# Performance work log

Hardware: AMD Instinct MI355X
Metric: run time of the kernel (lower is better)

## Reference

```python
import jax, jax.numpy as jnp
import numpy as np

L, H, D, FF, T, S, N = 4, 16, 1024, 4096, 256, 256, 16
NEG = -1e9

def layer_norm(x, g, b):
    mu = jnp.mean(x, axis=-1, keepdims=True)
    var = jnp.var(x, axis=-1, keepdims=True)
    return (x - mu) / jnp.sqrt(var + 1e-5) * g + b

def mha(q_in, k_in, v_in, wq, bq, wk, bk, wv, bv, wo, bo, mask):
    # q_in: [T,N,D]; k_in/v_in: [S,N,D]
    t, n, d = q_in.shape
    s = k_in.shape[0]
    hd = d // H
    scale = hd ** -0.5
    q = (q_in @ wq.T + bq) * scale
    k = k_in @ wk.T + bk
    v = v_in @ wv.T + bv
    q = q.reshape(t, n, H, hd)
    k = k.reshape(s, n, H, hd)
    v = v.reshape(s, n, H, hd)
    scores = jnp.einsum('tnhd,snhd->nhts', q, k)  # [N,H,T,S]
    if mask is not None:
        scores = scores + mask  # mask [T,S] broadcasts
    a = jax.nn.softmax(scores, axis=-1)
    o = jnp.einsum('nhts,snhd->tnhd', a, v).reshape(t, n, d)
    return o @ wo.T + bo

def forward(tgt, memory, sa_wq, sa_bq, sa_wk, sa_bk, sa_wv, sa_bv, sa_wo, sa_bo,
            ca_wq, ca_bq, ca_wk, ca_bk, ca_wv, ca_bv, ca_wo, ca_bo,
            w1, b1, w2, b2, ln1_g, ln1_b, ln2_g, ln2_b, ln3_g, ln3_b, lnf_g, lnf_b):
    t = tgt.shape[0]
    causal = jnp.where(jnp.triu(jnp.ones((t, t), bool), 1), jnp.float32(NEG), jnp.float32(0.0))
    x = tgt
    for i in range(L):
        sa = mha(x, x, x, sa_wq[i], sa_bq[i], sa_wk[i], sa_bk[i], sa_wv[i], sa_bv[i], sa_wo[i], sa_bo[i], causal)
        x = layer_norm(x + sa, ln1_g[i], ln1_b[i])
        ca = mha(x, memory, memory, ca_wq[i], ca_bq[i], ca_wk[i], ca_bk[i], ca_wv[i], ca_bv[i], ca_wo[i], ca_bo[i], None)
        x = layer_norm(x + ca, ln2_g[i], ln2_b[i])
        ff = jax.nn.relu(x @ w1[i].T + b1[i]) @ w2[i].T + b2[i]
        x = layer_norm(x + ff, ln3_g[i], ln3_b[i])
    return layer_norm(x, lnf_g, lnf_b)

def setup_inputs() -> dict:
    key = jax.random.key(0)
    ks = iter(jax.random.split(key, 40))
    def nrm(shape, s):
        return (jax.random.normal(next(ks), shape, jnp.float32) * s).astype(jnp.float32)
    sd = D ** -0.5
    inp = {
        'tgt': nrm((T, N, D), 1.0),
        'memory': nrm((S, N, D), 1.0),
    }
    for pre in ('sa', 'ca'):
        for nm in ('wq', 'wk', 'wv', 'wo'):
            inp[f'{pre}_{nm}'] = nrm((L, D, D), sd)
        for nm in ('bq', 'bk', 'bv', 'bo'):
            inp[f'{pre}_{nm}'] = jnp.zeros((L, D), jnp.float32)
    inp['w1'] = nrm((L, FF, D), sd)
    inp['b1'] = jnp.zeros((L, FF), jnp.float32)
    inp['w2'] = nrm((L, D, FF), FF ** -0.5)
    inp['b2'] = jnp.zeros((L, D), jnp.float32)
    for nm in ('ln1', 'ln2', 'ln3'):
        inp[f'{nm}_g'] = jnp.ones((L, D), jnp.float32)
        inp[f'{nm}_b'] = jnp.zeros((L, D), jnp.float32)
    inp['lnf_g'] = jnp.ones((D,), jnp.float32)
    inp['lnf_b'] = jnp.zeros((D,), jnp.float32)
    return inp

def reference(tgt, memory, sa_wq, sa_bq, sa_wk, sa_bk, sa_wv, sa_bv, sa_wo, sa_bo,
              ca_wq, ca_bq, ca_wk, ca_bk, ca_wv, ca_bv, ca_wo, ca_bo,
              w1, b1, w2, b2, ln1_g, ln1_b, ln2_g, ln2_b, ln3_g, ln3_b, lnf_g, lnf_b):
    return forward(tgt, memory, sa_wq, sa_bq, sa_wk, sa_bk, sa_wv, sa_bv, sa_wo, sa_bo,
                   ca_wq, ca_bq, ca_wk, ca_bk, ca_wv, ca_bv, ca_wo, ca_bo,
                   w1, b1, w2, b2, ln1_g, ln1_b, ln2_g, ln2_b, ln3_g, ln3_b, lnf_g, lnf_b)
```

## Files before the change

### kernel.cpp

```cpp
#include <hip/hip_runtime.h>


typedef __attribute__((ext_vector_type(4))) float f32x4;
typedef __attribute__((ext_vector_type(8))) short bf16x8;
typedef __attribute__((ext_vector_type(4))) unsigned short u16x4;
typedef __attribute__((ext_vector_type(4))) unsigned int   u32x4;

__device__ __forceinline__ unsigned short f2bf(float f) {
    unsigned int u = __builtin_bit_cast(unsigned int, f);
    u += 0x7fffu + ((u >> 16) & 1u);
    return (unsigned short)(u >> 16);
}

__device__ __forceinline__ void gll16(const unsigned short* g, unsigned short* l) {
    auto* gp = reinterpret_cast<const __attribute__((address_space(1))) unsigned int*>(
        reinterpret_cast<uintptr_t>(g));
    auto* lp = reinterpret_cast<__attribute__((address_space(3))) unsigned int*>(
        reinterpret_cast<uintptr_t>(l));
    __builtin_amdgcn_global_load_lds(gp, lp, 16, 0, 0);
}

__global__ __launch_bounds__(256, 4) void gemm128(
    const unsigned short* __restrict__ A,
    const unsigned short* __restrict__ Bw,
    const float* __restrict__ bias,
    unsigned short* __restrict__ outb,
    float* __restrict__ outf0,
    float* __restrict__ outf1,
    int N, int lda, int klen, int mode)
{
    __shared__ unsigned short Al[2][128 * 32];
    __shared__ unsigned short Bl[2][128 * 32];
    const int tid  = threadIdx.x;
    const int lane = tid & 63;
    const int w    = tid >> 6;
    const int wr   = (w >> 1) * 64;
    const int wc   = (w & 1) * 64;
    const int l15  = lane & 15;
    const int l4   = lane >> 4;

    const int gx   = gridDim.x;
    const int orig = blockIdx.y * gx + blockIdx.x;
    const int xcd  = orig & 7;
    const int lin  = orig >> 3;
    const int m0   = (xcd * 4 + (lin & 3)) * 128;
    const int n0   = (lin >> 2) * 128;
    const int kz   = blockIdx.z * klen;

    const int srow = w * 16 + (lane >> 2);
    const int scol = ((lane & 3) ^ ((srow >> 1) & 3)) * 8;
    const unsigned short* ag = A  + (size_t)(m0 + srow) * lda + kz + scol;
    const unsigned short* bg = Bw + (size_t)(n0 + srow) * lda + kz + scol;
    const size_t jstep = (size_t)64 * lda;
    const int lbase = (w * 16) * 32;

    int aoff[4], boff[4];
    #pragma unroll
    for (int i = 0; i < 4; ++i) {
        const int ra = wr + i * 16 + l15;
        const int rb = wc + i * 16 + l15;
        aoff[i] = ra * 32 + ((l4 ^ ((ra >> 1) & 3)) * 8);
        boff[i] = rb * 32 + ((l4 ^ ((rb >> 1) & 3)) * 8);
    }

    f32x4 acc[4][4];
    #pragma unroll
    for (int mi = 0; mi < 4; ++mi)
        #pragma unroll
        for (int ni = 0; ni < 4; ++ni)
            acc[mi][ni] = (f32x4){0.f, 0.f, 0.f, 0.f};

    #pragma unroll
    for (int j = 0; j < 2; ++j) {
        gll16(ag + j * jstep, &Al[0][lbase + j * 64 * 32]);
        gll16(bg + j * jstep, &Bl[0][lbase + j * 64 * 32]);
    }
    __syncthreads();

    const int nt = klen >> 5;
    int cur = 0;
    for (int t = 0; t < nt; ++t) {
        if (t + 1 < nt) {
            ag += 32; bg += 32;
            #pragma unroll
            for (int j = 0; j < 2; ++j) {
                gll16(ag + j * jstep, &Al[cur ^ 1][lbase + j * 64 * 32]);
                gll16(bg + j * jstep, &Bl[cur ^ 1][lbase + j * 64 * 32]);
            }
        }
        const unsigned short* ac = &Al[cur][0];
        const unsigned short* bc = &Bl[cur][0];
        bf16x8 af[4], bf[4];
        #pragma unroll
        for (int i = 0; i < 4; ++i) af[i] = *reinterpret_cast<const bf16x8*>(&ac[aoff[i]]);
        #pragma unroll
        for (int i = 0; i < 4; ++i) bf[i] = *reinterpret_cast<const bf16x8*>(&bc[boff[i]]);
        #pragma unroll
        for (int mi = 0; mi < 4; ++mi)
            #pragma unroll
            for (int ni = 0; ni < 4; ++ni)
                acc[mi][ni] = __builtin_amdgcn_mfma_f32_16x16x32_bf16(af[mi], bf[ni], acc[mi][ni], 0, 0, 0);
        __syncthreads();
        cur ^= 1;
    }

    float* po = (blockIdx.z == 0) ? outf0 : outf1;
    #pragma unroll
    for (int mi = 0; mi < 4; ++mi) {
        #pragma unroll
        for (int ni = 0; ni < 4; ++ni) {
            const int col = n0 + wc + ni * 16 + l15;
            const float bs = (mode == 3) ? 0.f : bias[col];
            #pragma unroll
            for (int r = 0; r < 4; ++r) {
                const int row = m0 + wr + mi * 16 + l4 * 4 + r;
                const float val = acc[mi][ni][r] + bs;
                if (mode == 0)      outb[(size_t)row * N + col] = f2bf(val);
                else if (mode == 1) outb[(size_t)row * N + col] = f2bf(fmaxf(val, 0.f));
                else                po[(size_t)row * N + col] = val;
            }
        }
    }
}

__global__ __launch_bounds__(256) void gemm_bt64(
    const unsigned short* __restrict__ A,
    const unsigned short* __restrict__ Bw,
    const float* __restrict__ bias,
    const float* __restrict__ resid,
    unsigned short* __restrict__ outb,
    float* __restrict__ outf,
    int M, int N, int K, int mode)
{
    __shared__ unsigned short Al[2][64 * 32];
    __shared__ unsigned short Bl[2][128 * 32];
    const int tid  = threadIdx.x;
    const int lane = tid & 63;
    const int w    = tid >> 6;
    const int wr   = (w >> 1) * 32;
    const int wc   = (w & 1) * 64;
    const int l15  = lane & 15;
    const int l4   = lane >> 4;

    const int gx = gridDim.x;
    const int orig = blockIdx.y * gx + blockIdx.x;
    const int xcd  = orig & 7;
    const int lin  = orig >> 3;
    const int m0   = (xcd * 8 + (lin & 7)) * 64;
    const int n0   = (lin >> 3) * 128;

    const int srow = w * 16 + (lane >> 2);
    const int scol = ((lane & 3) ^ ((srow >> 1) & 3)) * 8;
    const unsigned short* ag = A  + (size_t)(m0 + srow) * K + scol;
    const unsigned short* bg = Bw + (size_t)(n0 + srow) * K + scol;
    const size_t jstep = (size_t)64 * K;
    const int lbase = (w * 16) * 32;

    int aoff[2], boff[4];
    #pragma unroll
    for (int i = 0; i < 2; ++i) {
        const int ra = wr + i * 16 + l15;
        aoff[i] = ra * 32 + ((l4 ^ ((ra >> 1) & 3)) * 8);
    }
    #pragma unroll
    for (int i = 0; i < 4; ++i) {
        const int rb = wc + i * 16 + l15;
        boff[i] = rb * 32 + ((l4 ^ ((rb >> 1) & 3)) * 8);
    }

    f32x4 acc[2][4];
    #pragma unroll
    for (int mi = 0; mi < 2; ++mi)
        #pragma unroll
        for (int ni = 0; ni < 4; ++ni)
            acc[mi][ni] = (f32x4){0.f, 0.f, 0.f, 0.f};

    gll16(ag, &Al[0][lbase]);
    #pragma unroll
    for (int j = 0; j < 2; ++j) gll16(bg + j * jstep, &Bl[0][lbase + j * 64 * 32]);
    __syncthreads();

    const int nt = K >> 5;
    int cur = 0;
    for (int t = 0; t < nt; ++t) {
        if (t + 1 < nt) {
            ag += 32; bg += 32;
            gll16(ag, &Al[cur ^ 1][lbase]);
            #pragma unroll
            for (int j = 0; j < 2; ++j) gll16(bg + j * jstep, &Bl[cur ^ 1][lbase + j * 64 * 32]);
        }
        const unsigned short* ac = &Al[cur][0];
        const unsigned short* bc = &Bl[cur][0];
        bf16x8 af[2], bf[4];
        #pragma unroll
        for (int i = 0; i < 2; ++i) af[i] = *reinterpret_cast<const bf16x8*>(&ac[aoff[i]]);
        #pragma unroll
        for (int i = 0; i < 4; ++i) bf[i] = *reinterpret_cast<const bf16x8*>(&bc[boff[i]]);
        #pragma unroll
        for (int mi = 0; mi < 2; ++mi)
            #pragma unroll
            for (int ni = 0; ni < 4; ++ni)
                acc[mi][ni] = __builtin_amdgcn_mfma_f32_16x16x32_bf16(af[mi], bf[ni], acc[mi][ni], 0, 0, 0);
        __syncthreads();
        cur ^= 1;
    }

    #pragma unroll
    for (int mi = 0; mi < 2; ++mi) {
        #pragma unroll
        for (int ni = 0; ni < 4; ++ni) {
            const int col = n0 + wc + ni * 16 + l15;
            const float bs = bias[col];
            #pragma unroll
            for (int r = 0; r < 4; ++r) {
                const int row = m0 + wr + mi * 16 + l4 * 4 + r;
                const float val = acc[mi][ni][r] + bs;
                if (mode == 0) outb[(size_t)row * N + col] = f2bf(val);
                else           outf[(size_t)row * N + col] = val + resid[(size_t)row * N + col];
            }
        }
    }
}

__global__ __launch_bounds__(256) void attn_fused(
    const unsigned short* __restrict__ Q, int qs,
    const unsigned short* __restrict__ Kb, int ks_,
    const unsigned short* __restrict__ Vb, int vs,
    unsigned short* __restrict__ O,
    int causal)
{
    __shared__ unsigned short Kl[8][256][8];
    __shared__ unsigned short Vt[32][64][8];
    __shared__ unsigned short Pl[4][32][16][8];
    const int tid  = threadIdx.x;
    const int lane = tid & 63;
    const int w    = tid >> 6;
    const int n    = blockIdx.x >> 4;
    const int h    = blockIdx.x & 15;
    const int l15  = lane & 15;
    const int l4   = lane >> 4;
    const size_t hoff = (size_t)h * 64;

    #pragma unroll
    for (int i = 0; i < 8; ++i) {
        const int e = i * 256 + tid;
        const int s = e >> 3;
        const int c = e & 7;
        u32x4 kv = *reinterpret_cast<const u32x4*>(&Kb[((size_t)s * 16 + n) * ks_ + hoff + c * 8]);
        *reinterpret_cast<u32x4*>(&Kl[c][s][0]) = kv;
        u32x4 vv = *reinterpret_cast<const u32x4*>(&Vb[((size_t)s * 16 + n) * vs + hoff + c * 8]);
        const unsigned short* ve = reinterpret_cast<const unsigned short*>(&vv);
        #pragma unroll
        for (int j = 0; j < 8; ++j)
            Vt[s >> 3][c * 8 + j][s & 7] = ve[j];
    }
    __syncthreads();

    for (int ch = 0; ch < 4; ++ch) {
        const int t0 = w * 64 + ch * 16;
        bf16x8 qa[2];
        #pragma unroll
        for (int ks = 0; ks < 2; ++ks)
            qa[ks] = *reinterpret_cast<const bf16x8*>(
                &Q[((size_t)(t0 + l15) * 16 + n) * qs + hoff + ks * 32 + l4 * 8]);

        f32x4 sc[16];
        #pragma unroll
        for (int st = 0; st < 16; ++st) {
            f32x4 a = (f32x4){0.f, 0.f, 0.f, 0.f};
            #pragma unroll
            for (int ks = 0; ks < 2; ++ks) {
                bf16x8 kf = *reinterpret_cast<const bf16x8*>(&Kl[ks * 4 + l4][st * 16 + l15][0]);
                a = __builtin_amdgcn_mfma_f32_16x16x32_bf16(qa[ks], kf, a, 0, 0, 0);
            }
            sc[st] = a;
        }
        if (causal) {
            #pragma unroll
            for (int st = 0; st < 16; ++st) {
                const int sg = st * 16 + l15;
                #pragma unroll
                for (int r = 0; r < 4; ++r) {
                    const int tg = t0 + l4 * 4 + r;
                    if (sg > tg) sc[st][r] += -1e9f;
                }
            }
        }
        #pragma unroll
        for (int r = 0; r < 4; ++r) {
            float mx = -3.0e38f;
            #pragma unroll
            for (int st = 0; st < 16; ++st) mx = fmaxf(mx, sc[st][r]);
            #pragma unroll
            for (int dd = 1; dd < 16; dd <<= 1) mx = fmaxf(mx, __shfl_xor(mx, dd, 64));
            float sum = 0.f;
            #pragma unroll
            for (int st = 0; st < 16; ++st) {
                const float e = __expf(sc[st][r] - mx);
                sc[st][r] = e;
                sum += e;
            }
            #pragma unroll
            for (int dd = 1; dd < 16; dd <<= 1) sum += __shfl_xor(sum, dd, 64);
            const float inv = 1.f / sum;
            const int rl = l4 * 4 + r;
            #pragma unroll
            for (int st = 0; st < 16; ++st) {
                const int sg = st * 16 + l15;
                Pl[w][sg >> 3][rl][sg & 7] = f2bf(sc[st][r] * inv);
            }
        }
        f32x4 oacc[4];
        #pragma unroll
        for (int dt = 0; dt < 4; ++dt) oacc[dt] = (f32x4){0.f, 0.f, 0.f, 0.f};
        #pragma unroll
        for (int kt = 0; kt < 8; ++kt) {
            bf16x8 pa = *reinterpret_cast<const bf16x8*>(&Pl[w][kt * 4 + l4][l15][0]);
            #pragma unroll
            for (int dt = 0; dt < 4; ++dt) {
                bf16x8 vf = *reinterpret_cast<const bf16x8*>(&Vt[kt * 4 + l4][dt * 16 + l15][0]);
                oacc[dt] = __builtin_amdgcn_mfma_f32_16x16x32_bf16(pa, vf, oacc[dt], 0, 0, 0);
            }
        }
        #pragma unroll
        for (int dt = 0; dt < 4; ++dt)
            #pragma unroll
            for (int r = 0; r < 4; ++r)
                O[((size_t)(t0 + l4 * 4 + r) * 16 + n) * 1024 + hoff + dt * 16 + l15] = f2bf(oacc[dt][r]);
    }
}

__device__ __forceinline__ void ln_body(
    f32x4 (&v)[4], int row, int lane,
    const float* __restrict__ g, const float* __restrict__ b,
    float* __restrict__ xf, unsigned short* __restrict__ xb)
{
    float s = 0.f;
    #pragma unroll
    for (int i = 0; i < 4; ++i) s += v[i][0] + v[i][1] + v[i][2] + v[i][3];
    #pragma unroll
    for (int dd = 1; dd < 64; dd <<= 1) s += __shfl_xor(s, dd, 64);
    const float mu = s * (1.f / 1024.f);
    float q = 0.f;
    #pragma unroll
    for (int i = 0; i < 4; ++i)
        #pragma unroll
        for (int j = 0; j < 4; ++j) { const float d0 = v[i][j] - mu; q += d0 * d0; }
    #pragma unroll
    for (int dd = 1; dd < 64; dd <<= 1) q += __shfl_xor(q, dd, 64);
    const float rstd = rsqrtf(q * (1.f / 1024.f) + 1e-5f);
    #pragma unroll
    for (int i = 0; i < 4; ++i) {
        const int col = i * 256 + lane * 4;
        f32x4 gg = *reinterpret_cast<const f32x4*>(&g[col]);
        f32x4 bb = *reinterpret_cast<const f32x4*>(&b[col]);
        f32x4 y;
        #pragma unroll
        for (int j = 0; j < 4; ++j) y[j] = (v[i][j] - mu) * rstd * gg[j] + bb[j];
        if (xf) *reinterpret_cast<f32x4*>(&xf[(size_t)row * 1024 + col]) = y;
        if (xb) {
            u16x4 pk;
            #pragma unroll
            for (int j = 0; j < 4; ++j) pk[j] = f2bf(y[j]);
            *reinterpret_cast<u16x4*>(&xb[(size_t)row * 1024 + col]) = pk;
        }
    }
}

__global__ __launch_bounds__(256) void ln_kernel(
    const float* __restrict__ z, const float* __restrict__ g, const float* __restrict__ b,
    float* __restrict__ xf, unsigned short* __restrict__ xb)
{
    const int row  = blockIdx.x * 4 + (threadIdx.x >> 6);
    const int lane = threadIdx.x & 63;
    f32x4 v[4];
    #pragma unroll
    for (int i = 0; i < 4; ++i)
        v[i] = *reinterpret_cast<const f32x4*>(&z[(size_t)row * 1024 + i * 256 + lane * 4]);
    ln_body(v, row, lane, g, b, xf, xb);
}

__global__ __launch_bounds__(256) void ln_red2(
    const float* __restrict__ p0, const float* __restrict__ p1,
    const float* __restrict__ bias, const float* __restrict__ resid,
    const float* __restrict__ g, const float* __restrict__ b,
    float* __restrict__ xf, unsigned short* __restrict__ xb)
{
    const int row  = blockIdx.x * 4 + (threadIdx.x >> 6);
    const int lane = threadIdx.x & 63;
    f32x4 v[4];
    #pragma unroll
    for (int i = 0; i < 4; ++i) {
        const int col = i * 256 + lane * 4;
        const size_t o = (size_t)row * 1024 + col;
        f32x4 a0 = *reinterpret_cast<const f32x4*>(&p0[o]);
        f32x4 a1 = *reinterpret_cast<const f32x4*>(&p1[o]);
        f32x4 bs = *reinterpret_cast<const f32x4*>(&bias[col]);
        f32x4 rs = *reinterpret_cast<const f32x4*>(&resid[o]);
        v[i] = a0 + a1 + bs + rs;
    }
    ln_body(v, row, lane, g, b, xf, xb);
}

__global__ __launch_bounds__(256) void cvt_bf16(
    const float* __restrict__ in, unsigned short* __restrict__ out, int n)
{
    const int i = (blockIdx.x * 256 + threadIdx.x) * 4;
    if (i >= n) return;
    f32x4 v = *reinterpret_cast<const f32x4*>(&in[i]);
    u16x4 pk;
    #pragma unroll
    for (int j = 0; j < 4; ++j) pk[j] = f2bf(v[j]);
    *reinterpret_cast<u16x4*>(&out[i]) = pk;
}

__global__ __launch_bounds__(256) void pack_layer_w(
    const float* __restrict__ sa_wq, const float* __restrict__ sa_wk, const float* __restrict__ sa_wv,
    const float* __restrict__ ca_wq, const float* __restrict__ ca_wk, const float* __restrict__ ca_wv,
    const float* __restrict__ sa_wo, const float* __restrict__ ca_wo,
    const float* __restrict__ w1,   const float* __restrict__ w2,
    unsigned short* __restrict__ dst, int layer)
{
    const size_t DD = 1024u * 1024u;
    const size_t e  = ((size_t)blockIdx.x * 256 + threadIdx.x) * 4;
    const float* src;
    float scale = 1.f;
    if (e < 3 * DD) {
        const int part = (int)(e / DD);
        src = (part == 0 ? sa_wq : part == 1 ? sa_wk : sa_wv) + layer * DD + (e % DD);
        if (part == 0) scale = 0.125f;
    } else if (e < 6 * DD) {
        const size_t r = e - 3 * DD;
        const int part = (int)(r / DD);
        src = (part == 0 ? ca_wq : part == 1 ? ca_wk : ca_wv) + layer * DD + (r % DD);
        if (part == 0) scale = 0.125f;
    } else if (e < 7 * DD)  { src = sa_wo + layer * DD + (e - 6 * DD); }
    else if (e < 8 * DD)    { src = ca_wo + layer * DD + (e - 7 * DD); }
    else if (e < 12 * DD)   { src = w1 + (size_t)layer * 4 * DD + (e - 8 * DD); }
    else                    { src = w2 + (size_t)layer * 4 * DD + (e - 12 * DD); }
    f32x4 v = *reinterpret_cast<const f32x4*>(src);
    u16x4 pk;
    #pragma unroll
    for (int j = 0; j < 4; ++j) pk[j] = f2bf(v[j] * scale);
    *reinterpret_cast<u16x4*>(&dst[e]) = pk;
}

__global__ __launch_bounds__(256) void pack_bias(
    const float* __restrict__ sa_bq, const float* __restrict__ sa_bk, const float* __restrict__ sa_bv,
    const float* __restrict__ ca_bq, const float* __restrict__ ca_bk, const float* __restrict__ ca_bv,
    float* __restrict__ sab, float* __restrict__ cab)
{
    const int idx = blockIdx.x * 256 + threadIdx.x;
    const int half = idx / 12288;
    const int r    = idx % 12288;
    const int l    = r / 3072;
    const int pc   = r % 3072;
    const int part = pc >> 10;
    const int c    = pc & 1023;
    const float* src = half == 0 ? (part == 0 ? sa_bq : part == 1 ? sa_bk : sa_bv)
                                 : (part == 0 ? ca_bq : part == 1 ? ca_bk : ca_bv);
    const float v = src[l * 1024 + c] * (part == 0 ? 0.125f : 1.f);
    (half ? cab : sab)[l * 3072 + pc] = v;
}

extern "C" void kernel_launch(void* const* d_in, const int* in_sizes, int n_in,
                              void* d_out, int out_size, void* d_ws, size_t ws_size,
                              hipStream_t stream)
{
    (void)in_sizes; (void)n_in; (void)out_size; (void)ws_size;
    const int M  = 4096;
    const int Dm = 1024;
    const size_t DD = (size_t)Dm * Dm;

    const float* tgt   = (const float*)d_in[0];
    const float* mem   = (const float*)d_in[1];
    const float* sa_wq = (const float*)d_in[2];
    const float* sa_wk = (const float*)d_in[3];
    const float* sa_wv = (const float*)d_in[4];
    const float* sa_wo = (const float*)d_in[5];
    const float* sa_bq = (const float*)d_in[6];
    const float* sa_bk = (const float*)d_in[7];
    const float* sa_bv = (const float*)d_in[8];
    const float* sa_bo = (const float*)d_in[9];
    const float* ca_wq = (const float*)d_in[10];
    const float* ca_wk = (const float*)d_in[11];
    const float* ca_wv = (const float*)d_in[12];
    const float* ca_wo = (const float*)d_in[13];
    const float* ca_bq = (const float*)d_in[14];
    const float* ca_bk = (const float*)d_in[15];
    const float* ca_bv = (const float*)d_in[16];
    const float* ca_bo = (const float*)d_in[17];
    const float* w1    = (const float*)d_in[18];
    const float* b1    = (const float*)d_in[19];
    const float* w2    = (const float*)d_in[20];
    const float* b2    = (const float*)d_in[21];
    const float* ln1g  = (const float*)d_in[22];
    const float* ln1b  = (const float*)d_in[23];
    const float* ln2g  = (const float*)d_in[24];
    const float* ln2b  = (const float*)d_in[25];
    const float* ln3g  = (const float*)d_in[26];
    const float* ln3b  = (const float*)d_in[27];
    const float* lnfg  = (const float*)d_in[28];
    const float* lnfb  = (const float*)d_in[29];

    char* p = (char*)d_ws;
    float*          x_f    = (float*)p;          p += (size_t)M * Dm * 4;
    unsigned short* x_b    = (unsigned short*)p; p += (size_t)M * Dm * 2;
    unsigned short* mem_b  = (unsigned short*)p; p += (size_t)M * Dm * 2;
    unsigned short* qkv_b  = (unsigned short*)p; p += (size_t)M * 3072 * 2;
    unsigned short* cakv_b = (unsigned short*)p; p += (size_t)M * 2048 * 2;
    unsigned short* caq_b  = (unsigned short*)p; p += (size_t)M * Dm * 2;
    unsigned short* ao_b   = (unsigned short*)p; p += (size_t)M * Dm * 2;
    unsigned short* wpack  = (unsigned short*)p; p += 16 * DD * 2;
    float*          sab    = (float*)p;          p += 4 * 3072 * 4;
    float*          cab    = (float*)p;          p += 4 * 3072 * 4;
    unsigned short* h_b    = qkv_b;
    float*          par0   = (float*)((char*)qkv_b + (size_t)M * 4096 * 2);
    float*          par1   = (float*)wpack;
    float*          z_f    = (float*)d_out;

    dim3 blk(256);
    auto gemm64 = [&](const unsigned short* A, const unsigned short* Bw, const float* bias,
                      const float* resid, unsigned short* ob, float* of, int N, int K, int mode) {
        dim3 grid(N / 128, M / 64);
        gemm_bt64<<<grid, blk, 0, stream>>>(A, Bw, bias, resid, ob, of, M, N, K, mode);
    };

    cvt_bf16<<<4096, blk, 0, stream>>>(tgt, x_b, M * Dm);
    cvt_bf16<<<4096, blk, 0, stream>>>(mem, mem_b, M * Dm);
    pack_bias<<<96, blk, 0, stream>>>(sa_bq, sa_bk, sa_bv, ca_bq, ca_bk, ca_bv, sab, cab);

    const float* res = tgt;
    for (int i = 0; i < 4; ++i) {
        pack_layer_w<<<16384, blk, 0, stream>>>(sa_wq, sa_wk, sa_wv, ca_wq, ca_wk, ca_wv,
                                                sa_wo, ca_wo, w1, w2, wpack, i);
        gemm128<<<dim3(24, 32, 1), blk, 0, stream>>>(x_b, wpack, sab + i * 3072,
            qkv_b, nullptr, nullptr, 3072, 1024, 1024, 0);
        attn_fused<<<256, blk, 0, stream>>>(qkv_b, 3072, qkv_b + 1024, 3072, qkv_b + 2048, 3072, ao_b, 1);
        gemm64(ao_b, wpack + 6 * DD, sa_bo + i * Dm, res, nullptr, z_f, 1024, 1024, 2);
        ln_kernel<<<1024, blk, 0, stream>>>(z_f, ln1g + i * Dm, ln1b + i * Dm, x_f, x_b);
        res = x_f;
        gemm64(x_b, wpack + 3 * DD, cab + i * 3072, nullptr, caq_b, nullptr, 1024, 1024, 0);
        gemm128<<<dim3(16, 32, 1), blk, 0, stream>>>(mem_b, wpack + 4 * DD, cab + i * 3072 + 1024,
            cakv_b, nullptr, nullptr, 2048, 1024, 1024, 0);
        attn_fused<<<256, blk, 0, stream>>>(caq_b, 1024, cakv_b, 2048, cakv_b + 1024, 2048, ao_b, 0);
        gemm64(ao_b, wpack + 7 * DD, ca_bo + i * Dm, x_f, nullptr, z_f, 1024, 1024, 2);
        ln_kernel<<<1024, blk, 0, stream>>>(z_f, ln2g + i * Dm, ln2b + i * Dm, x_f, x_b);
        gemm128<<<dim3(32, 32, 1), blk, 0, stream>>>(x_b, wpack + 8 * DD, b1 + i * 4096,
            h_b, nullptr, nullptr, 4096, 1024, 1024, 1);
        gemm128<<<dim3(8, 32, 2), blk, 0, stream>>>(h_b, wpack + 12 * DD, nullptr,
            nullptr, par0, par1, 1024, 4096, 2048, 3);
        ln_red2<<<1024, blk, 0, stream>>>(par0, par1, b2 + i * Dm, x_f,
            ln3g + i * Dm, ln3b + i * Dm, x_f, x_b);
    }
    ln_kernel<<<1024, blk, 0, stream>>>(x_f, lnfg, lnfb, (float*)d_out, nullptr);
}
```

Baseline: 1.358 ms.

## Split attention over query halves, skip masked tiles, fuse cross-attn projections

Attention now launches twice as many 128-thread blocks, each covering half the query rows, and causal self-attention skips score and PV tiles that lie entirely above the diagonal. The cross-attention Q and KV projections are merged into one grouped GEMM launch. The output projections use the 128-tile GEMM with split-K into two partial buffers, reduced inside ln_red2 together with bias, residual and layer norm. This removes the separate 64-row GEMM and the standalone layer-norm kernels, which cuts launches and exposes more parallelism, at the cost of extra partial-sum traffic and each attention block reloading the full K/V.

```diff
diff --git a/kernel.cpp b/kernel.cpp
--- a/kernel.cpp
+++ b/kernel.cpp
@@ -18,6 +18,99 @@
     auto* lp = reinterpret_cast<__attribute__((address_space(3))) unsigned int*>(
         reinterpret_cast<uintptr_t>(l));
     __builtin_amdgcn_global_load_lds(gp, lp, 16, 0, 0);
+}
+
+__device__ __forceinline__ void gemm_body(
+    const unsigned short* __restrict__ A,
+    const unsigned short* __restrict__ Bw,
+    const float* __restrict__ bias,
+    unsigned short* __restrict__ outb,
+    float* __restrict__ po,
+    int N, int lda, int klen, int mode,
+    int m0, int n0, int kz,
+    unsigned short (*Al)[128 * 32], unsigned short (*Bl)[128 * 32])
+{
+    const int tid  = threadIdx.x;
+    const int lane = tid & 63;
+    const int w    = tid >> 6;
+    const int wr   = (w >> 1) * 64;
+    const int wc   = (w & 1) * 64;
+    const int l15  = lane & 15;
+    const int l4   = lane >> 4;
+
+    const int srow = w * 16 + (lane >> 2);
+    const int scol = ((lane & 3) ^ ((srow >> 1) & 3)) * 8;
+    const unsigned short* ag = A  + (size_t)(m0 + srow) * lda + kz + scol;
+    const unsigned short* bg = Bw + (size_t)(n0 + srow) * lda + kz + scol;
+    const size_t jstep = (size_t)64 * lda;
+    const int lbase = (w * 16) * 32;
+
+    int aoff[4], boff[4];
+    #pragma unroll
+    for (int i = 0; i < 4; ++i) {
+        const int ra = wr + i * 16 + l15;
+        const int rb = wc + i * 16 + l15;
+        aoff[i] = ra * 32 + ((l4 ^ ((ra >> 1) & 3)) * 8);
+        boff[i] = rb * 32 + ((l4 ^ ((rb >> 1) & 3)) * 8);
+    }
+
+    f32x4 acc[4][4];
+    #pragma unroll
+    for (int mi = 0; mi < 4; ++mi)
+        #pragma unroll
+        for (int ni = 0; ni < 4; ++ni)
+            acc[mi][ni] = (f32x4){0.f, 0.f, 0.f, 0.f};
+
+    #pragma unroll
+    for (int j = 0; j < 2; ++j) {
+        gll16(ag + j * jstep, &Al[0][lbase + j * 64 * 32]);
+        gll16(bg + j * jstep, &Bl[0][lbase + j * 64 * 32]);
+    }
+    __syncthreads();
+
+    const int nt = klen >> 5;
+    int cur = 0;
+    for (int t = 0; t < nt; ++t) {
+        if (t + 1 < nt) {
+            ag += 32; bg += 32;
+            #pragma unroll
+            for (int j = 0; j < 2; ++j) {
+                gll16(ag + j * jstep, &Al[cur ^ 1][lbase + j * 64 * 32]);
+                gll16(bg + j * jstep, &Bl[cur ^ 1][lbase + j * 64 * 32]);
+            }
+        }
+        const unsigned short* ac = &Al[cur][0];
+        const unsigned short* bc = &Bl[cur][0];
+        bf16x8 af[4], bf[4];
+        #pragma unroll
+        for (int i = 0; i < 4; ++i) af[i] = *reinterpret_cast<const bf16x8*>(&ac[aoff[i]]);
+        #pragma unroll
+        for (int i = 0; i < 4; ++i) bf[i] = *reinterpret_cast<const bf16x8*>(&bc[boff[i]]);
+        #pragma unroll
+        for (int mi = 0; mi < 4; ++mi)
+            #pragma unroll
+            for (int ni = 0; ni < 4; ++ni)
+                acc[mi][ni] = __builtin_amdgcn_mfma_f32_16x16x32_bf16(af[mi], bf[ni], acc[mi][ni], 0, 0, 0);
+        __syncthreads();
+        cur ^= 1;
+    }
+
+    #pragma unroll
+    for (int mi = 0; mi < 4; ++mi) {
+        #pragma unroll
+        for (int ni = 0; ni < 4; ++ni) {
+            const int col = n0 + wc + ni * 16 + l15;
+            const float bs = (mode == 3) ? 0.f : bias[col];
+            #pragma unroll
+            for (int r = 0; r < 4; ++r) {
+                const int row = m0 + wr + mi * 16 + l4 * 4 + r;
+                const float val = acc[mi][ni][r] + bs;
+                if (mode == 0)      outb[(size_t)row * N + col] = f2bf(val);
+                else if (mode == 1) outb[(size_t)row * N + col] = f2bf(fmaxf(val, 0.f));
+                else                po[(size_t)row * N + col] = val;
+            }
+        }
+    }
 }
 
 __global__ __launch_bounds__(256, 4) void gemm128(
@@ -31,14 +124,6 @@
 {
     __shared__ unsigned short Al[2][128 * 32];
     __shared__ unsigned short Bl[2][128 * 32];
-    const int tid  = threadIdx.x;
-    const int lane = tid & 63;
-    const int w    = tid >> 6;
-    const int wr   = (w >> 1) * 64;
-    const int wc   = (w & 1) * 64;
-    const int l15  = lane & 15;
-    const int l4   = lane >> 4;
-
     const int gx   = gridDim.x;
     const int orig = blockIdx.y * gx + blockIdx.x;
     const int xcd  = orig & 7;
@@ -46,183 +131,33 @@
     const int m0   = (xcd * 4 + (lin & 3)) * 128;
     const int n0   = (lin >> 2) * 128;
     const int kz   = blockIdx.z * klen;
-
-    const int srow = w * 16 + (lane >> 2);
-    const int scol = ((lane & 3) ^ ((srow >> 1) & 3)) * 8;
-    const unsigned short* ag = A  + (size_t)(m0 + srow) * lda + kz + scol;
-    const unsigned short* bg = Bw + (size_t)(n0 + srow) * lda + kz + scol;
-    const size_t jstep = (size_t)64 * lda;
-    const int lbase = (w * 16) * 32;
-
-    int aoff[4], boff[4];
-    #pragma unroll
-    for (int i = 0; i < 4; ++i) {
-        const int ra = wr + i * 16 + l15;
-        const int rb = wc + i * 16 + l15;
-        aoff[i] = ra * 32 + ((l4 ^ ((ra >> 1) & 3)) * 8);
-        boff[i] = rb * 32 + ((l4 ^ ((rb >> 1) & 3)) * 8);
-    }
-
-    f32x4 acc[4][4];
-    #pragma unroll
-    for (int mi = 0; mi < 4; ++mi)
-        #pragma unroll
-        for (int ni = 0; ni < 4; ++ni)
-            acc[mi][ni] = (f32x4){0.f, 0.f, 0.f, 0.f};
-
-    #pragma unroll
-    for (int j = 0; j < 2; ++j) {
-        gll16(ag + j * jstep, &Al[0][lbase + j * 64 * 32]);
-        gll16(bg + j * jstep, &Bl[0][lbase + j * 64 * 32]);
-    }
-    __syncthreads();
-
-    const int nt = klen >> 5;
-    int cur = 0;
-    for (int t = 0; t < nt; ++t) {
-        if (t + 1 < nt) {
-            ag += 32; bg += 32;
-            #pragma unroll
-            for (int j = 0; j < 2; ++j) {
-                gll16(ag + j * jstep, &Al[cur ^ 1][lbase + j * 64 * 32]);
-                gll16(bg + j * jstep, &Bl[cur ^ 1][lbase + j * 64 * 32]);
-            }
-        }
-        const unsigned short* ac = &Al[cur][0];
-        const unsigned short* bc = &Bl[cur][0];
-        bf16x8 af[4], bf[4];
-        #pragma unroll
-        for (int i = 0; i < 4; ++i) af[i] = *reinterpret_cast<const bf16x8*>(&ac[aoff[i]]);
-        #pragma unroll
-        for (int i = 0; i < 4; ++i) bf[i] = *reinterpret_cast<const bf16x8*>(&bc[boff[i]]);
-        #pragma unroll
-        for (int mi = 0; mi < 4; ++mi)
-            #pragma unroll
-            for (int ni = 0; ni < 4; ++ni)
-                acc[mi][ni] = __builtin_amdgcn_mfma_f32_16x16x32_bf16(af[mi], bf[ni], acc[mi][ni], 0, 0, 0);
-        __syncthreads();
-        cur ^= 1;
-    }
-
     float* po = (blockIdx.z == 0) ? outf0 : outf1;
-    #pragma unroll
-    for (int mi = 0; mi < 4; ++mi) {
-        #pragma unroll
-        for (int ni = 0; ni < 4; ++ni) {
-            const int col = n0 + wc + ni * 16 + l15;
-            const float bs = (mode == 3) ? 0.f : bias[col];
-            #pragma unroll
-            for (int r = 0; r < 4; ++r) {
-                const int row = m0 + wr + mi * 16 + l4 * 4 + r;
-                const float val = acc[mi][ni][r] + bs;
-                if (mode == 0)      outb[(size_t)row * N + col] = f2bf(val);
-                else if (mode == 1) outb[(size_t)row * N + col] = f2bf(fmaxf(val, 0.f));
-                else                po[(size_t)row * N + col] = val;
-            }
-        }
-    }
-}
-
-__global__ __launch_bounds__(256) void gemm_bt64(
-    const unsigned short* __restrict__ A,
-    const unsigned short* __restrict__ Bw,
-    const float* __restrict__ bias,
-    const float* __restrict__ resid,
-    unsigned short* __restrict__ outb,
-    float* __restrict__ outf,
-    int M, int N, int K, int mode)
-{
-    __shared__ unsigned short Al[2][64 * 32];
+    gemm_body(A, Bw, bias, outb, po, N, lda, klen, mode, m0, n0, kz, Al, Bl);
+}
+
+__global__ __launch_bounds__(256, 4) void gemm128_ca(
+    const unsigned short* __restrict__ A0, const unsigned short* __restrict__ A1,
+    const unsigned short* __restrict__ B0, const unsigned short* __restrict__ B1,
+    const float* __restrict__ bias0, const float* __restrict__ bias1,
+    unsigned short* __restrict__ out0, unsigned short* __restrict__ out1,
+    int lda, int klen)
+{
+    __shared__ unsigned short Al[2][128 * 32];
     __shared__ unsigned short Bl[2][128 * 32];
-    const int tid  = threadIdx.x;
-    const int lane = tid & 63;
-    const int w    = tid >> 6;
-    const int wr   = (w >> 1) * 32;
-    const int wc   = (w & 1) * 64;
-    const int l15  = lane & 15;
-    const int l4   = lane >> 4;
-
-    const int gx = gridDim.x;
-    const int orig = blockIdx.y * gx + blockIdx.x;
+    const int grp = (blockIdx.x >= 8);
+    const int bx  = blockIdx.x - (grp ? 8 : 0);
+    const int lgx = grp ? 16 : 8;
+    const int orig = blockIdx.y * lgx + bx;
     const int xcd  = orig & 7;
     const int lin  = orig >> 3;
-    const int m0   = (xcd * 8 + (lin & 7)) * 64;
-    const int n0   = (lin >> 3) * 128;
-
-    const int srow = w * 16 + (lane >> 2);
-    const int scol = ((lane & 3) ^ ((srow >> 1) & 3)) * 8;
-    const unsigned short* ag = A  + (size_t)(m0 + srow) * K + scol;
-    const unsigned short* bg = Bw + (size_t)(n0 + srow) * K + scol;
-    const size_t jstep = (size_t)64 * K;
-    const int lbase = (w * 16) * 32;
-
-    int aoff[2], boff[4];
-    #pragma unroll
-    for (int i = 0; i < 2; ++i) {
-        const int ra = wr + i * 16 + l15;
-        aoff[i] = ra * 32 + ((l4 ^ ((ra >> 1) & 3)) * 8);
-    }
-    #pragma unroll
-    for (int i = 0; i < 4; ++i) {
-        const int rb = wc + i * 16 + l15;
-        boff[i] = rb * 32 + ((l4 ^ ((rb >> 1) & 3)) * 8);
-    }
-
-    f32x4 acc[2][4];
-    #pragma unroll
-    for (int mi = 0; mi < 2; ++mi)
-        #pragma unroll
-        for (int ni = 0; ni < 4; ++ni)
-            acc[mi][ni] = (f32x4){0.f, 0.f, 0.f, 0.f};
-
-    gll16(ag, &Al[0][lbase]);
-    #pragma unroll
-    for (int j = 0; j < 2; ++j) gll16(bg + j * jstep, &Bl[0][lbase + j * 64 * 32]);
-    __syncthreads();
-
-    const int nt = K >> 5;
-    int cur = 0;
-    for (int t = 0; t < nt; ++t) {
-        if (t + 1 < nt) {
-            ag += 32; bg += 32;
-            gll16(ag, &Al[cur ^ 1][lbase]);
-            #pragma unroll
-            for (int j = 0; j < 2; ++j) gll16(bg + j * jstep, &Bl[cur ^ 1][lbase + j * 64 * 32]);
-        }
-        const unsigned short* ac = &Al[cur][0];
-        const unsigned short* bc = &Bl[cur][0];
-        bf16x8 af[2], bf[4];
-        #pragma unroll
-        for (int i = 0; i < 2; ++i) af[i] = *reinterpret_cast<const bf16x8*>(&ac[aoff[i]]);
-        #pragma unroll
-        for (int i = 0; i < 4; ++i) bf[i] = *reinterpret_cast<const bf16x8*>(&bc[boff[i]]);
-        #pragma unroll
-        for (int mi = 0; mi < 2; ++mi)
-            #pragma unroll
-            for (int ni = 0; ni < 4; ++ni)
-                acc[mi][ni] = __builtin_amdgcn_mfma_f32_16x16x32_bf16(af[mi], bf[ni], acc[mi][ni], 0, 0, 0);
-        __syncthreads();
-        cur ^= 1;
-    }
-
-    #pragma unroll
-    for (int mi = 0; mi < 2; ++mi) {
-        #pragma unroll
-        for (int ni = 0; ni < 4; ++ni) {
-            const int col = n0 + wc + ni * 16 + l15;
-            const float bs = bias[col];
-            #pragma unroll
-            for (int r = 0; r < 4; ++r) {
-                const int row = m0 + wr + mi * 16 + l4 * 4 + r;
-                const float val = acc[mi][ni][r] + bs;
-                if (mode == 0) outb[(size_t)row * N + col] = f2bf(val);
-                else           outf[(size_t)row * N + col] = val + resid[(size_t)row * N + col];
-            }
-        }
-    }
-}
-
-__global__ __launch_bounds__(256) void attn_fused(
+    const int m0   = (xcd * 4 + (lin & 3)) * 128;
+    const int n0   = (lin >> 2) * 128;
+    gemm_body(grp ? A1 : A0, grp ? B1 : B0, grp ? bias1 : bias0,
+              grp ? out1 : out0, nullptr, grp ? 2048 : 1024, lda, klen, 0,
+              m0, n0, 0, Al, Bl);
+}
+
+__global__ __launch_bounds__(128) void attn_fused(
     const unsigned short* __restrict__ Q, int qs,
     const unsigned short* __restrict__ Kb, int ks_,
     const unsigned short* __restrict__ Vb, int vs,
@@ -231,19 +166,21 @@
 {
     __shared__ unsigned short Kl[8][256][8];
     __shared__ unsigned short Vt[32][64][8];
-    __shared__ unsigned short Pl[4][32][16][8];
-    const int tid  = threadIdx.x;
-    const int lane = tid & 63;
-    const int w    = tid >> 6;
-    const int n    = blockIdx.x >> 4;
-    const int h    = blockIdx.x & 15;
-    const int l15  = lane & 15;
-    const int l4   = lane >> 4;
+    __shared__ unsigned short Pl[2][32][16][8];
+    const int tid   = threadIdx.x;
+    const int lane  = tid & 63;
+    const int w     = tid >> 6;
+    const int bxi   = blockIdx.x;
+    const int n     = bxi >> 5;
+    const int h     = (bxi >> 1) & 15;
+    const int thalf = bxi & 1;
+    const int l15   = lane & 15;
+    const int l4    = lane >> 4;
     const size_t hoff = (size_t)h * 64;
 
     #pragma unroll
-    for (int i = 0; i < 8; ++i) {
-        const int e = i * 256 + tid;
+    for (int i = 0; i < 16; ++i) {
+        const int e = i * 128 + tid;
         const int s = e >> 3;
         const int c = e & 7;
         u32x4 kv = *reinterpret_cast<const u32x4*>(&Kb[((size_t)s * 16 + n) * ks_ + hoff + c * 8]);
@@ -257,7 +194,7 @@
     __syncthreads();
 
     for (int ch = 0; ch < 4; ++ch) {
-        const int t0 = w * 64 + ch * 16;
+        const int t0 = thalf * 128 + w * 64 + ch * 16;
         bf16x8 qa[2];
         #pragma unroll
         for (int ks = 0; ks < 2; ++ks)
@@ -267,6 +204,10 @@
         f32x4 sc[16];
         #pragma unroll
         for (int st = 0; st < 16; ++st) {
+            if (causal && st * 16 > t0 + 15) {
+                sc[st] = (f32x4){-1e9f, -1e9f, -1e9f, -1e9f};
+                continue;
+            }
             f32x4 a = (f32x4){0.f, 0.f, 0.f, 0.f};
             #pragma unroll
             for (int ks = 0; ks < 2; ++ks) {
@@ -282,7 +223,7 @@
                 #pragma unroll
                 for (int r = 0; r < 4; ++r) {
                     const int tg = t0 + l4 * 4 + r;
-                    if (sg > tg) sc[st][r] += -1e9f;
+                    if (sg > tg) sc[st][r] = -1e9f;
                 }
             }
         }
@@ -315,6 +256,7 @@
         for (int dt = 0; dt < 4; ++dt) oacc[dt] = (f32x4){0.f, 0.f, 0.f, 0.f};
         #pragma unroll
         for (int kt = 0; kt < 8; ++kt) {
+            if (causal && kt * 32 > t0 + 15) continue;
             bf16x8 pa = *reinterpret_cast<const bf16x8*>(&Pl[w][kt * 4 + l4][l15][0]);
             #pragma unroll
             for (int dt = 0; dt < 4; ++dt) {
@@ -515,16 +457,12 @@
     float*          sab    = (float*)p;          p += 4 * 3072 * 4;
     float*          cab    = (float*)p;          p += 4 * 3072 * 4;
     unsigned short* h_b    = qkv_b;
+    float*          parA   = (float*)qkv_b;
+    float*          parB   = (float*)cakv_b;
     float*          par0   = (float*)((char*)qkv_b + (size_t)M * 4096 * 2);
     float*          par1   = (float*)wpack;
-    float*          z_f    = (float*)d_out;
-
-    dim3 blk(256);
-    auto gemm64 = [&](const unsigned short* A, const unsigned short* Bw, const float* bias,
-                      const float* resid, unsigned short* ob, float* of, int N, int K, int mode) {
-        dim3 grid(N / 128, M / 64);
-        gemm_bt64<<<grid, blk, 0, stream>>>(A, Bw, bias, resid, ob, of, M, N, K, mode);
-    };
+
+    dim3 blk(256), blkA(128);
 
     cvt_bf16<<<4096, blk, 0, stream>>>(tgt, x_b, M * Dm);
     cvt_bf16<<<4096, blk, 0, stream>>>(mem, mem_b, M * Dm);
@@ -536,16 +474,21 @@
                                                 sa_wo, ca_wo, w1, w2, wpack, i);
         gemm128<<<dim3(24, 32, 1), blk, 0, stream>>>(x_b, wpack, sab + i * 3072,
             qkv_b, nullptr, nullptr, 3072, 1024, 1024, 0);
-        attn_fused<<<256, blk, 0, stream>>>(qkv_b, 3072, qkv_b + 1024, 3072, qkv_b + 2048, 3072, ao_b, 1);
-        gemm64(ao_b, wpack + 6 * DD, sa_bo + i * Dm, res, nullptr, z_f, 1024, 1024, 2);
-        ln_kernel<<<1024, blk, 0, stream>>>(z_f, ln1g + i * Dm, ln1b + i * Dm, x_f, x_b);
+        attn_fused<<<512, blkA, 0, stream>>>(qkv_b, 3072, qkv_b + 1024, 3072, qkv_b + 2048, 3072, ao_b, 1);
+        gemm128<<<dim3(8, 32, 2), blk, 0, stream>>>(ao_b, wpack + 6 * DD, nullptr,
+            nullptr, parA, parB, 1024, 1024, 512, 3);
+        ln_red2<<<1024, blk, 0, stream>>>(parA, parB, sa_bo + i * Dm, res,
+            ln1g + i * Dm, ln1b + i * Dm, x_f, x_b);
         res = x_f;
-        gemm64(x_b, wpack + 3 * DD, cab + i * 3072, nullptr, caq_b, nullptr, 1024, 1024, 0);
-        gemm128<<<dim3(16, 32, 1), blk, 0, stream>>>(mem_b, wpack + 4 * DD, cab + i * 3072 + 1024,
-            cakv_b, nullptr, nullptr, 2048, 1024, 1024, 0);
-        attn_fused<<<256, blk, 0, stream>>>(caq_b, 1024, cakv_b, 2048, cakv_b + 1024, 2048, ao_b, 0);
-        gemm64(ao_b, wpack + 7 * DD, ca_bo + i * Dm, x_f, nullptr, z_f, 1024, 1024, 2);
-        ln_kernel<<<1024, blk, 0, stream>>>(z_f, ln2g + i * Dm, ln2b + i * Dm, x_f, x_b);
+        gemm128_ca<<<dim3(24, 32, 1), blk, 0, stream>>>(x_b, mem_b,
+            wpack + 3 * DD, wpack + 4 * DD,
+            cab + i * 3072, cab + i * 3072 + 1024,
+            caq_b, cakv_b, 1024, 1024);
+        attn_fused<<<512, blkA, 0, stream>>>(caq_b, 1024, cakv_b, 2048, cakv_b + 1024, 2048, ao_b, 0);
+        gemm128<<<dim3(8, 32, 2), blk, 0, stream>>>(ao_b, wpack + 7 * DD, nullptr,
+            nullptr, parA, parB, 1024, 1024, 512, 3);
+        ln_red2<<<1024, blk, 0, stream>>>(parA, parB, ca_bo + i * Dm, x_f,
+            ln2g + i * Dm, ln2b + i * Dm, x_f, x_b);
         gemm128<<<dim3(32, 32, 1), blk, 0, stream>>>(x_b, wpack + 8 * DD, b1 + i * 4096,
             h_b, nullptr, nullptr, 4096, 1024, 1024, 1);
         gemm128<<<dim3(8, 32, 2), blk, 0, stream>>>(h_b, wpack + 12 * DD, nullptr,
```

Result: faster. 1.323 ms (-2.6%).
